# Optimization experiments

Measured on AMD Instinct MI355X. Metric: run time of the kernel, lower is better.

Reference implementation:

```python
import math
import jax, jax.numpy as jnp
import numpy as np

D = 512        # encoder_dim
LLM = 4096     # llm_dim
H = 8          # heads
L = 2          # depth
FF = 4 * D     # feedforward hidden
DH = D // H    # head dim
EPS = 1e-5


def setup_inputs() -> dict:
    key = jax.random.key(0)
    ks = jax.random.split(key, 16)
    s_d = 1.0 / math.sqrt(D)
    s_ff = 1.0 / math.sqrt(FF)
    inp = {
        "x": jax.random.normal(ks[0], (1, 8192, D), dtype=jnp.float32),
        # per-layer params, leading dim L
        "ln1_g": jnp.ones((L, D), jnp.float32),
        "ln1_b": jnp.zeros((L, D), jnp.float32),
        "Wq": jax.random.normal(ks[1], (L, D, D), jnp.float32) * s_d,
        "Wk": jax.random.normal(ks[2], (L, D, D), jnp.float32) * s_d,
        "Wv": jax.random.normal(ks[3], (L, D, D), jnp.float32) * s_d,
        "Wo": jax.random.normal(ks[4], (L, D, D), jnp.float32) * s_d,
        "bo": jnp.zeros((L, D), jnp.float32),
        "ln2_g": jnp.ones((L, D), jnp.float32),
        "ln2_b": jnp.zeros((L, D), jnp.float32),
        "W1": jax.random.normal(ks[5], (L, D, FF), jnp.float32) * s_d,
        "b1": jnp.zeros((L, FF), jnp.float32),
        "W2": jax.random.normal(ks[6], (L, FF, D), jnp.float32) * s_ff,
        "b2": jnp.zeros((L, D), jnp.float32),
        # final projector (xavier-like)
        "proj_W": jax.random.normal(ks[7], (D, LLM), jnp.float32) * math.sqrt(2.0 / (D + LLM)),
        "proj_b": jnp.zeros((LLM,), jnp.float32),
    }
    return inp


def _layernorm(h, g, b):
    mu = jnp.mean(h, axis=-1, keepdims=True)
    var = jnp.var(h, axis=-1, keepdims=True)
    return (h - mu) * jax.lax.rsqrt(var + EPS) * g + b


def _sinusoidal_pe(n, d):
    pos = jnp.arange(n, dtype=jnp.float32)[:, None]
    div = jnp.exp(jnp.arange(0, d, 2, dtype=jnp.float32) * (-math.log(10000.0) / d))
    pe = jnp.zeros((n, d), jnp.float32)
    pe = pe.at[:, 0::2].set(jnp.sin(pos * div))
    pe = pe.at[:, 1::2].set(jnp.cos(pos * div))
    return pe


def reference(x, ln1_g, ln1_b, Wq, Wk, Wv, Wo, bo, ln2_g, ln2_b, W1, b1, W2, b2, proj_W, proj_b):
    B, N, _ = x.shape
    x = x + _sinusoidal_pe(N, D)[None]  # positional encoding (dropout = identity at eval)
    scale = DH ** -0.5
    for l in range(L):
        # --- linear self-attention block (PreNorm + residual) ---
        h = _layernorm(x, ln1_g[l], ln1_b[l])
        q = (h @ Wq[l]).reshape(B, N, H, DH).transpose(0, 2, 1, 3)  # bhnd
        k = (h @ Wk[l]).reshape(B, N, H, DH).transpose(0, 2, 1, 3)
        v = (h @ Wv[l]).reshape(B, N, H, DH).transpose(0, 2, 1, 3)
        q = jax.nn.softmax(q, axis=-1) * scale        # softmax over feature dim
        k = jax.nn.softmax(k, axis=-2)                # softmax over sequence dim
        ctx = jnp.einsum('bhnd,bhne->bhde', k, v)     # small [B,H,DH,DH] context
        o = jnp.einsum('bhnd,bhde->bhne', q, ctx)
        o = o.transpose(0, 2, 1, 3).reshape(B, N, D)
        x = x + (o @ Wo[l] + bo[l])
        # --- feedforward block (PreNorm + residual, exact GELU) ---
        h = _layernorm(x, ln2_g[l], ln2_b[l])
        x = x + (jax.nn.gelu(h @ W1[l] + b1[l], approximate=False) @ W2[l] + b2[l])
    x = jnp.squeeze(x, 0)  # batch==1, matches torch x.squeeze(0)
    return x @ proj_W + proj_b  # [N, LLM]
```

## Files before the change

### kernel.cpp

```cpp
#include <hip/hip_runtime.h>
#include <hip/hip_bf16.h>
#include <math.h>

constexpr int N_SEQ = 8192;
constexpr int D     = 512;
constexpr int NH    = 8;
constexpr int FFDIM = 2048;
constexpr int LLMD  = 4096;
constexpr int NLAYER= 2;

typedef __bf16 bf16x8 __attribute__((ext_vector_type(8)));
typedef float  f32x4  __attribute__((ext_vector_type(4)));
typedef unsigned short u16x8 __attribute__((ext_vector_type(8)));

__device__ __forceinline__ unsigned short f2bf(float x) {
  unsigned u = __builtin_bit_cast(unsigned, x);
  unsigned r = (u + 0x7FFFu + ((u >> 16) & 1u)) >> 16;
  return (unsigned short)r;
}
__device__ __forceinline__ float bf2f(unsigned short u) {
  unsigned x = ((unsigned)u) << 16;
  return __builtin_bit_cast(float, x);
}

#define GLOAD16(g, l)                                                        \
  __builtin_amdgcn_global_load_lds(                                          \
      (const __attribute__((address_space(1))) void*)(g),                    \
      (__attribute__((address_space(3))) void*)(l), 16, 0, 0)

__global__ __launch_bounds__(256) void prep_kernel(const float* __restrict__ Wq,
                                                   const float* __restrict__ Wk,
                                                   const float* __restrict__ Wv,
                                                   const float* __restrict__ Wo,
                                                   const float* __restrict__ W1,
                                                   const float* __restrict__ W2,
                                                   const float* __restrict__ Wp,
                                                   unsigned short* __restrict__ WT,
                                                   const float* __restrict__ xin,
                                                   float* __restrict__ X,
                                                   unsigned short* __restrict__ Hb,
                                                   const float* __restrict__ g,
                                                   const float* __restrict__ b) {
  int bid = blockIdx.x;
  if (bid >= 8192) {
    int row  = ((bid - 8192) * 256 + (int)threadIdx.x) >> 6;
    int lane = threadIdx.x & 63;
    const float* p = xin + (size_t)row * D + lane * 8;
    float x[8];
#pragma unroll
    for (int i = 0; i < 8; ++i) {
      int d = lane * 8 + i;
      float freq = __expf((float)(d & ~1) * (-9.210340371976184f / 512.0f));
      float arg = (float)row * freq;
      float pe = (d & 1) ? cosf(arg) : sinf(arg);
      x[i] = p[i] + pe;
    }
    float s = 0.f, sq = 0.f;
#pragma unroll
    for (int i = 0; i < 8; ++i) { s += x[i]; sq += x[i] * x[i]; }
#pragma unroll
    for (int o = 32; o > 0; o >>= 1) { s += __shfl_xor(s, o); sq += __shfl_xor(sq, o); }
    float mu  = s * (1.0f / D);
    float var = sq * (1.0f / D) - mu * mu;
    float rs  = rsqrtf(var + 1e-5f);
    float* Xp = X + (size_t)row * D + lane * 8;
    u16x8 r;
#pragma unroll
    for (int i = 0; i < 8; ++i) {
      Xp[i] = x[i];
      r[i] = f2bf((x[i] - mu) * rs * g[lane * 8 + i] + b[lane * 8 + i]);
    }
    *(u16x8*)(Hb + (size_t)row * D + lane * 8) = r;
    return;
  }
  const float* src; unsigned short* dst; int K, N, tile;
  if (bid < 2048) {
    int mat = bid >> 8; int w = mat >> 1, l = mat & 1;
    const float* s4 = (w == 0) ? Wq : (w == 1) ? Wk : (w == 2) ? Wv : Wo;
    src = s4 + (size_t)l * 262144;
    dst = WT + ((size_t)l * 4 + w) * 262144;
    K = 512; N = 512; tile = bid & 255;
  } else if (bid < 4096) {
    int b2 = bid - 2048; int l = b2 >> 10;
    src = W1 + (size_t)l * 1048576; dst = WT + 2097152 + (size_t)l * 1048576;
    K = 512; N = 2048; tile = b2 & 1023;
  } else if (bid < 6144) {
    int b2 = bid - 4096; int l = b2 >> 10;
    src = W2 + (size_t)l * 1048576; dst = WT + 4194304 + (size_t)l * 1048576;
    K = 2048; N = 512; tile = b2 & 1023;
  } else {
    src = Wp; dst = WT + 6291456; K = 512; N = 4096; tile = bid - 6144;
  }
  int tilesN = N >> 5;
  int bk = (tile / tilesN) << 5, bn = (tile % tilesN) << 5;
  __shared__ float s[32][33];
  int r = threadIdx.x >> 5, c = threadIdx.x & 31;
#pragma unroll
  for (int i = 0; i < 4; ++i)
    s[r + 8 * i][c] = src[(size_t)(bk + r + 8 * i) * N + bn + c];
  __syncthreads();
#pragma unroll
  for (int i = 0; i < 4; ++i) {
    int rr = r + 8 * i;
    dst[(size_t)(bn + rr) * K + bk + c] = f2bf(s[c][rr]);
  }
}

__global__ __launch_bounds__(256) void ln_bf16(const float* __restrict__ in,
                                               unsigned short* __restrict__ out,
                                               const float* __restrict__ g,
                                               const float* __restrict__ b) {
  int row  = (blockIdx.x * 256 + threadIdx.x) >> 6;
  int lane = threadIdx.x & 63;
  const float* p = in + (size_t)row * D + lane * 8;
  f32x4 v0 = *(const f32x4*)p;
  f32x4 v1 = *(const f32x4*)(p + 4);
  float s  = v0[0] + v0[1] + v0[2] + v0[3] + v1[0] + v1[1] + v1[2] + v1[3];
  float sq = v0[0]*v0[0] + v0[1]*v0[1] + v0[2]*v0[2] + v0[3]*v0[3]
           + v1[0]*v1[0] + v1[1]*v1[1] + v1[2]*v1[2] + v1[3]*v1[3];
#pragma unroll
  for (int o = 32; o > 0; o >>= 1) { s += __shfl_xor(s, o); sq += __shfl_xor(sq, o); }
  float mu  = s * (1.0f / D);
  float var = sq * (1.0f / D) - mu * mu;
  float rs  = rsqrtf(var + 1e-5f);
  f32x4 g0 = *(const f32x4*)(g + lane * 8);
  f32x4 g1 = *(const f32x4*)(g + lane * 8 + 4);
  f32x4 b0 = *(const f32x4*)(b + lane * 8);
  f32x4 b1 = *(const f32x4*)(b + lane * 8 + 4);
  u16x8 r;
#pragma unroll
  for (int i = 0; i < 4; ++i) r[i]     = f2bf((v0[i] - mu) * rs * g0[i] + b0[i]);
#pragma unroll
  for (int i = 0; i < 4; ++i) r[i + 4] = f2bf((v1[i] - mu) * rs * g1[i] + b1[i]);
  *(u16x8*)(out + (size_t)row * D + lane * 8) = r;
}

template <int FLAGS, int BN>
__global__ __launch_bounds__(256) void mgemm2(const unsigned short* __restrict__ A,
                                              const unsigned short* __restrict__ Bt,
                                              const float* __restrict__ bias,
                                              const float* __restrict__ res,
                                              float* __restrict__ C,
                                              unsigned short* __restrict__ Cb,
                                              int M, int N, int K) {
  constexpr int WNI = BN / 32;
  __shared__ unsigned short As[4][128][32];
  __shared__ unsigned short Bs[4][BN][32];
  const int tid = threadIdx.x;
  const int lane = tid & 63, wv = tid >> 6;
  const int nwg = gridDim.x * gridDim.y;
  int bid = blockIdx.y * gridDim.x + blockIdx.x;
  bid = (bid & 7) * (nwg >> 3) + (bid >> 3);
  const int bm = (bid / gridDim.x) * 128, bn = (bid % gridDim.x) * BN;
  const int wr = (wv >> 1) * 64, wc = (wv & 1) * (BN / 2);
  f32x4 acc[4][WNI] = {};

  const int srA = wv * 32 + (lane >> 2);
  const int sc  = (lane & 3) * 8;
  const unsigned short* Ap0 = A + (size_t)(bm + srA) * K + sc;
  const unsigned short* Ap1 = Ap0 + (size_t)16 * K;
  const int srB = wv * (BN / 4) + (lane >> 2);
  const unsigned short* Bp0 = Bt + (size_t)(bn + srB) * K + sc;
  const unsigned short* Bp1 = Bp0 + (size_t)16 * K;
  const int kh = (lane >> 4) * 8;
  const int fr = lane & 15;

  auto stage = [&](int bb, int k0) {
    GLOAD16(Ap0 + k0, &As[bb][srA][sc]);
    GLOAD16(Ap1 + k0, &As[bb][srA + 16][sc]);
    GLOAD16(Bp0 + k0, &Bs[bb][srB][sc]);
    if constexpr (BN == 128) GLOAD16(Bp1 + k0, &Bs[bb][srB + 16][sc]);
  };

  const int nt = K >> 5;
  stage(0, 0);
  stage(1, 32);
  stage(2, 64);
  for (int t = 0; t < nt; ++t) {
    __builtin_amdgcn_sched_barrier(0);
    if constexpr (BN == 128)
      asm volatile("s_waitcnt vmcnt(8)" ::: "memory");
    else
      asm volatile("s_waitcnt vmcnt(6)" ::: "memory");
    __builtin_amdgcn_s_barrier();
    __builtin_amdgcn_sched_barrier(0);
    const int bb = t & 3;
    bf16x8 af[4], bfv[WNI];
#pragma unroll
    for (int mi = 0; mi < 4; ++mi)
      af[mi] = *(const bf16x8*)&As[bb][wr + mi * 16 + fr][kh];
#pragma unroll
    for (int ni = 0; ni < WNI; ++ni)
      bfv[ni] = *(const bf16x8*)&Bs[bb][wc + ni * 16 + fr][kh];
    if (t + 3 < nt) stage((t + 3) & 3, (t + 3) << 5);
#pragma unroll
    for (int mi = 0; mi < 4; ++mi)
#pragma unroll
      for (int ni = 0; ni < WNI; ++ni)
        acc[mi][ni] = __builtin_amdgcn_mfma_f32_16x16x32_bf16(af[mi], bfv[ni], acc[mi][ni], 0, 0, 0);
  }

  const int r4 = (lane >> 4) * 4, cc = lane & 15;
#pragma unroll
  for (int mi = 0; mi < 4; ++mi) {
#pragma unroll
    for (int ni = 0; ni < WNI; ++ni) {
      int col = bn + wc + ni * 16 + cc;
      float bsv = (FLAGS & 1) ? bias[col] : 0.0f;
      f32x4 v = acc[mi][ni];
#pragma unroll
      for (int j = 0; j < 4; ++j) {
        int row = bm + wr + mi * 16 + r4 + j;
        float x = v[j] + bsv;
        if (FLAGS & 2) x = 0.5f * x * (1.0f + erff(x * 0.7071067811865475f));
        if (FLAGS & 4) x += res[(size_t)row * N + col];
        if (!(FLAGS & 16)) C[(size_t)row * N + col] = x;
        if (FLAGS & 8) Cb[(size_t)row * N + col] = f2bf(x);
      }
    }
  }
}

__global__ __launch_bounds__(256) void qkv_gemm(const unsigned short* __restrict__ A,
                                                const unsigned short* __restrict__ Bt,
                                                unsigned short* __restrict__ Qb,
                                                unsigned short* __restrict__ Kb,
                                                unsigned short* __restrict__ Vb,
                                                float* __restrict__ pm,
                                                float* __restrict__ ps) {
  constexpr int K = 512;
  __shared__ unsigned short As[4][128][32];
  __shared__ unsigned short Bs[4][128][32];
  const int tid = threadIdx.x;
  const int lane = tid & 63, wv = tid >> 6;
  const int bm = blockIdx.y * 128, bn = blockIdx.x * 128;
  const int wr = (wv >> 1) * 64, wc = (wv & 1) * 64;
  f32x4 acc[4][4] = {};

  const int srA = wv * 32 + (lane >> 2);
  const int sc  = (lane & 3) * 8;
  const unsigned short* Ap0 = A + (size_t)(bm + srA) * K + sc;
  const unsigned short* Ap1 = Ap0 + (size_t)16 * K;
  const unsigned short* Bp0 = Bt + (size_t)(bn + srA) * K + sc;
  const unsigned short* Bp1 = Bp0 + (size_t)16 * K;
  const int kh = (lane >> 4) * 8;
  const int fr = lane & 15;

  auto stage = [&](int bb, int k0) {
    GLOAD16(Ap0 + k0, &As[bb][srA][sc]);
    GLOAD16(Ap1 + k0, &As[bb][srA + 16][sc]);
    GLOAD16(Bp0 + k0, &Bs[bb][srA][sc]);
    GLOAD16(Bp1 + k0, &Bs[bb][srA + 16][sc]);
  };

  stage(0, 0);
  stage(1, 32);
  stage(2, 64);
  for (int t = 0; t < 16; ++t) {
    __builtin_amdgcn_sched_barrier(0);
    asm volatile("s_waitcnt vmcnt(8)" ::: "memory");
    __builtin_amdgcn_s_barrier();
    __builtin_amdgcn_sched_barrier(0);
    const int bb = t & 3;
    bf16x8 af[4], bfv[4];
#pragma unroll
    for (int mi = 0; mi < 4; ++mi)
      af[mi] = *(const bf16x8*)&As[bb][wr + mi * 16 + fr][kh];
#pragma unroll
    for (int ni = 0; ni < 4; ++ni)
      bfv[ni] = *(const bf16x8*)&Bs[bb][wc + ni * 16 + fr][kh];
    if (t + 3 < 16) stage((t + 3) & 3, (t + 3) << 5);
#pragma unroll
    for (int mi = 0; mi < 4; ++mi)
#pragma unroll
      for (int ni = 0; ni < 4; ++ni)
        acc[mi][ni] = __builtin_amdgcn_mfma_f32_16x16x32_bf16(af[mi], bfv[ni], acc[mi][ni], 0, 0, 0);
  }

  const int r4 = (lane >> 4) * 4, cc = lane & 15;
  if (bn < 512) {
#pragma unroll
    for (int mi = 0; mi < 4; ++mi) {
#pragma unroll
      for (int j = 0; j < 4; ++j) {
        float v0 = acc[mi][0][j], v1 = acc[mi][1][j];
        float v2 = acc[mi][2][j], v3 = acc[mi][3][j];
        float m = fmaxf(fmaxf(v0, v1), fmaxf(v2, v3));
        m = fmaxf(m, __shfl_xor(m, 1)); m = fmaxf(m, __shfl_xor(m, 2));
        m = fmaxf(m, __shfl_xor(m, 4)); m = fmaxf(m, __shfl_xor(m, 8));
        float e0 = __expf(v0 - m), e1 = __expf(v1 - m);
        float e2 = __expf(v2 - m), e3 = __expf(v3 - m);
        float s = e0 + e1 + e2 + e3;
        s += __shfl_xor(s, 1); s += __shfl_xor(s, 2);
        s += __shfl_xor(s, 4); s += __shfl_xor(s, 8);
        float w = 0.125f / s;
        int row = bm + wr + mi * 16 + r4 + j;
        unsigned short* qr = Qb + (size_t)row * 512 + bn + wc + cc;
        qr[0] = f2bf(e0 * w); qr[16] = f2bf(e1 * w);
        qr[32] = f2bf(e2 * w); qr[48] = f2bf(e3 * w);
      }
    }
  } else if (bn < 1024) {
    int colb = bn - 512 + wc + cc;
    int prow = blockIdx.y * 2 + (wr ? 1 : 0);
#pragma unroll
    for (int ni = 0; ni < 4; ++ni) {
      float kf[4][4];
      float m = -1e30f;
#pragma unroll
      for (int mi = 0; mi < 4; ++mi)
#pragma unroll
        for (int j = 0; j < 4; ++j) {
          unsigned short kr = f2bf(acc[mi][ni][j]);
          Kb[(size_t)(bm + wr + mi * 16 + r4 + j) * 512 + colb + ni * 16] = kr;
          kf[mi][j] = bf2f(kr);
          m = fmaxf(m, kf[mi][j]);
        }
      m = fmaxf(m, __shfl_xor(m, 16));
      m = fmaxf(m, __shfl_xor(m, 32));
      float s = 0.f;
#pragma unroll
      for (int mi = 0; mi < 4; ++mi)
#pragma unroll
        for (int j = 0; j < 4; ++j) s += __expf(kf[mi][j] - m);
      s += __shfl_xor(s, 16);
      s += __shfl_xor(s, 32);
      if (lane < 16) {
        pm[(size_t)prow * 512 + colb + ni * 16] = m;
        ps[(size_t)prow * 512 + colb + ni * 16] = s;
      }
    }
  } else {
    int colv = bn - 1024 + wc + cc;
#pragma unroll
    for (int mi = 0; mi < 4; ++mi)
#pragma unroll
      for (int ni = 0; ni < 4; ++ni) {
        f32x4 v = acc[mi][ni];
#pragma unroll
        for (int j = 0; j < 4; ++j)
          Vb[(size_t)(bm + wr + mi * 16 + r4 + j) * 512 + colv + ni * 16] = f2bf(v[j]);
      }
  }
}

__global__ __launch_bounds__(256) void ctx_kernel(const unsigned short* __restrict__ kb,
                                                  const unsigned short* __restrict__ vb,
                                                  const float* __restrict__ pm,
                                                  const float* __restrict__ ps,
                                                  float* __restrict__ part) {
  int chunk = blockIdx.x, h = blockIdx.y, t = threadIdx.x;
  __shared__ float ks[64][64], vs[64][64];
  __shared__ float qm[4][64], qsum[4][64], scm[64], sci[64];
  {
    int c = t & 63, qt = t >> 6;
    float m = -1e30f, s = 0.f;
    for (int r = qt * 32; r < qt * 32 + 32; ++r) {
      float vm = pm[(size_t)r * 512 + h * 64 + c];
      float vp = ps[(size_t)r * 512 + h * 64 + c];
      float nm = fmaxf(m, vm);
      s = s * __expf(m - nm) + vp * __expf(vm - nm);
      m = nm;
    }
    qm[qt][c] = m; qsum[qt][c] = s;
  }
  __syncthreads();
  if (t < 64) {
    float M = fmaxf(fmaxf(qm[0][t], qm[1][t]), fmaxf(qm[2][t], qm[3][t]));
    float S = qsum[0][t] * __expf(qm[0][t] - M) + qsum[1][t] * __expf(qm[1][t] - M)
            + qsum[2][t] * __expf(qm[2][t] - M) + qsum[3][t] * __expf(qm[3][t] - M);
    scm[t] = M; sci[t] = 1.0f / S;
  }
  float acc[16] = {};
  int e0 = (t >> 6) * 16, dd = t & 63;
  for (int s0 = 0; s0 < 256; s0 += 64) {
    size_t rowbase = (size_t)chunk * 256 + s0;
    __syncthreads();
    for (int i = t; i < 1024; i += 256) {
      int r = i >> 4, c4 = (i & 15) * 4;
      ushort4 k4 = *(const ushort4*)&kb[(rowbase + r) * 512 + h * 64 + c4];
      ks[r][c4 + 0] = __expf(bf2f(k4.x) - scm[c4 + 0]) * sci[c4 + 0];
      ks[r][c4 + 1] = __expf(bf2f(k4.y) - scm[c4 + 1]) * sci[c4 + 1];
      ks[r][c4 + 2] = __expf(bf2f(k4.z) - scm[c4 + 2]) * sci[c4 + 2];
      ks[r][c4 + 3] = __expf(bf2f(k4.w) - scm[c4 + 3]) * sci[c4 + 3];
      ushort4 v4 = *(const ushort4*)&vb[(rowbase + r) * 512 + h * 64 + c4];
      vs[r][c4 + 0] = bf2f(v4.x); vs[r][c4 + 1] = bf2f(v4.y);
      vs[r][c4 + 2] = bf2f(v4.z); vs[r][c4 + 3] = bf2f(v4.w);
    }
    __syncthreads();
    for (int r = 0; r < 64; ++r) {
      float kd = ks[r][dd];
      float4 v0 = *(const float4*)&vs[r][e0];
      float4 v1 = *(const float4*)&vs[r][e0 + 4];
      float4 v2 = *(const float4*)&vs[r][e0 + 8];
      float4 v3 = *(const float4*)&vs[r][e0 + 12];
      acc[0]  = fmaf(kd, v0.x, acc[0]);  acc[1]  = fmaf(kd, v0.y, acc[1]);
      acc[2]  = fmaf(kd, v0.z, acc[2]);  acc[3]  = fmaf(kd, v0.w, acc[3]);
      acc[4]  = fmaf(kd, v1.x, acc[4]);  acc[5]  = fmaf(kd, v1.y, acc[5]);
      acc[6]  = fmaf(kd, v1.z, acc[6]);  acc[7]  = fmaf(kd, v1.w, acc[7]);
      acc[8]  = fmaf(kd, v2.x, acc[8]);  acc[9]  = fmaf(kd, v2.y, acc[9]);
      acc[10] = fmaf(kd, v2.z, acc[10]); acc[11] = fmaf(kd, v2.w, acc[11]);
      acc[12] = fmaf(kd, v3.x, acc[12]); acc[13] = fmaf(kd, v3.y, acc[13]);
      acc[14] = fmaf(kd, v3.z, acc[14]); acc[15] = fmaf(kd, v3.w, acc[15]);
    }
  }
  float* pb = &part[((size_t)h * 32 + chunk) * 4096 + dd * 64 + e0];
#pragma unroll
  for (int j = 0; j < 16; ++j) pb[j] = acc[j];
}

__global__ __launch_bounds__(256) void ctx_reduce_kernel(const float* __restrict__ part,
                                                         float* __restrict__ ctx) {
  int idx = blockIdx.x * 256 + threadIdx.x;
  int h = idx >> 12, de = idx & 4095;
  float s = 0.f;
#pragma unroll 8
  for (int c = 0; c < 32; ++c) s += part[((size_t)h * 32 + c) * 4096 + de];
  ctx[(size_t)h * 4096 + de] = s;
}

__global__ __launch_bounds__(256) void ctxw2_kernel(const float* __restrict__ ctx,
                                                    const float* __restrict__ Wo,
                                                    unsigned short* __restrict__ WPT) {
  int ct = blockIdx.x, h = blockIdx.y, t = threadIdx.x;
  __shared__ float cs[64][64];
  __shared__ float wo[64][64];
  for (int i = t; i < 4096; i += 256) {
    cs[i >> 6][i & 63] = ctx[(size_t)h * 4096 + i];
    wo[i >> 6][i & 63] = Wo[(size_t)(h * 64 + (i >> 6)) * 512 + ct * 64 + (i & 63)];
  }
  __syncthreads();
  int cl = t & 63, dg = (t >> 6) * 16;
  float accv[16];
#pragma unroll
  for (int j = 0; j < 16; ++j) accv[j] = 0.f;
  for (int e = 0; e < 64; ++e) {
    float w = wo[e][cl];
#pragma unroll
    for (int j = 0; j < 16; ++j) accv[j] = fmaf(cs[dg + j][e], w, accv[j]);
  }
  u16x8 o0, o1;
#pragma unroll
  for (int j = 0; j < 8; ++j) { o0[j] = f2bf(accv[j]); o1[j] = f2bf(accv[j + 8]); }
  unsigned short* dst = WPT + (size_t)(ct * 64 + cl) * 512 + h * 64 + dg;
  *(u16x8*)dst = o0;
  *(u16x8*)(dst + 8) = o1;
}

extern "C" void kernel_launch(void* const* d_in, const int* in_sizes, int n_in,
                              void* d_out, int out_size, void* d_ws, size_t ws_size,
                              hipStream_t stream) {
  const float* x_in  = (const float*)d_in[0];
  const float* ln1_g = (const float*)d_in[1];
  const float* ln1_b = (const float*)d_in[2];
  const float* Wq    = (const float*)d_in[3];
  const float* Wk    = (const float*)d_in[4];
  const float* Wv    = (const float*)d_in[5];
  const float* Wo    = (const float*)d_in[6];
  const float* bo    = (const float*)d_in[7];
  const float* ln2_g = (const float*)d_in[8];
  const float* ln2_b = (const float*)d_in[9];
  const float* W1    = (const float*)d_in[10];
  const float* b1    = (const float*)d_in[11];
  const float* W2    = (const float*)d_in[12];
  const float* b2    = (const float*)d_in[13];
  const float* projW = (const float*)d_in[14];
  const float* projb = (const float*)d_in[15];
  float* out = (float*)d_out;
  float* ws  = (float*)d_ws;
  constexpr size_t M1 = 1u << 20;

  float* X    = ws;
  float* CTXP = ws + 4 * M1;
  float* PM   = ws + 5 * M1;
  float* PS   = PM + 65536;
  float* CTX  = PS + 65536;
  unsigned short* Qb  = (unsigned short*)(ws + 6 * M1);
  unsigned short* Kb  = (unsigned short*)(ws + 8 * M1);
  unsigned short* Vb  = (unsigned short*)(ws + 10 * M1);
  unsigned short* Hb  = (unsigned short*)(ws + 12 * M1);
  unsigned short* Xb  = (unsigned short*)(ws + 14 * M1);
  unsigned short* FFH = (unsigned short*)(ws + 16 * M1);
  unsigned short* WT  = (unsigned short*)(ws + 24 * M1);
  unsigned short* WPT = (unsigned short*)(ws + 28 * M1);

  prep_kernel<<<10240, 256, 0, stream>>>(Wq, Wk, Wv, Wo, W1, W2, projW, WT,
                                         x_in, X, Hb, ln1_g, ln1_b);

  dim3 gqkv(1536 / 128, N_SEQ / 128);
  dim3 g512n(512 / 64, N_SEQ / 128);
  dim3 gff1(FFDIM / 128, N_SEQ / 128);
  dim3 gproj(LLMD / 128, N_SEQ / 128);

  for (int l = 0; l < NLAYER; ++l) {
    const unsigned short* WQKV = WT + (size_t)l * 1048576;
    const unsigned short* W1T  = WT + 2097152 + (size_t)l * 1048576;
    const unsigned short* W2T  = WT + 4194304 + (size_t)l * 1048576;

    qkv_gemm<<<gqkv, 256, 0, stream>>>(Hb, WQKV, Qb, Kb, Vb, PM, PS);
    ctx_kernel<<<dim3(32, NH), 256, 0, stream>>>(Kb, Vb, PM, PS, CTXP);
    ctx_reduce_kernel<<<128, 256, 0, stream>>>(CTXP, CTX);
    ctxw2_kernel<<<dim3(8, NH), 256, 0, stream>>>(CTX, Wo + (size_t)l * D * D, WPT);
    mgemm2<5, 64><<<g512n, 256, 0, stream>>>(Qb, WPT, bo + l * D, X, X, nullptr,
                                             N_SEQ, 512, 512);
    ln_bf16<<<N_SEQ / 4, 256, 0, stream>>>(X, Hb, ln2_g + l * D, ln2_b + l * D);
    mgemm2<27, 128><<<gff1, 256, 0, stream>>>(Hb, W1T, b1 + l * FFDIM, nullptr,
                                              nullptr, FFH, N_SEQ, FFDIM, 512);
    if (l == NLAYER - 1) {
      mgemm2<29, 64><<<g512n, 256, 0, stream>>>(FFH, W2T, b2 + l * D, X, nullptr,
                                                Xb, N_SEQ, 512, 2048);
    } else {
      mgemm2<5, 64><<<g512n, 256, 0, stream>>>(FFH, W2T, b2 + l * D, X, X, nullptr,
                                               N_SEQ, 512, 2048);
      ln_bf16<<<N_SEQ / 4, 256, 0, stream>>>(X, Hb, ln1_g + (l + 1) * D,
                                             ln1_b + (l + 1) * D);
    }
  }
  mgemm2<1, 128><<<gproj, 256, 0, stream>>>(Xb, WT + 6291456, projb, nullptr,
                                            out, nullptr, N_SEQ, LLMD, 512);
}
```

Measured before the change: 409.3 us.

## Use MFMA for ctx kernel and swizzle block order in qkv GEMM

The ctx kernel stages a whole 256-row chunk of softmaxed K and V into LDS as transposed, XOR-swizzled bf16 tiles. It then computes the 64x64 context with bf16 MFMA instructions instead of scalar fp32 FMAs. This replaces the fp32 LDS tiles and the loop of four staging steps with a single staging pass. Separately, the qkv_gemm block index is remapped so that workgroups are interleaved across eight groups, aiming for better cache or XCD locality. The softmaxed K is now rounded to bf16 before the product, which adds a small precision loss.

After: 383.5 us. 6.3% less time.

```diff
diff --git a/kernel.cpp b/kernel.cpp
--- a/kernel.cpp
+++ b/kernel.cpp
@@ -233,7 +233,11 @@
   __shared__ unsigned short Bs[4][128][32];
   const int tid = threadIdx.x;
   const int lane = tid & 63, wv = tid >> 6;
-  const int bm = blockIdx.y * 128, bn = blockIdx.x * 128;
+  const int nwg = gridDim.x * gridDim.y;
+  int bid = blockIdx.y * gridDim.x + blockIdx.x;
+  bid = (bid & 7) * (nwg >> 3) + (bid >> 3);
+  const int bm = (bid / gridDim.x) * 128, bn = (bid % gridDim.x) * 128;
+  const int bmy = bid / gridDim.x;
   const int wr = (wv >> 1) * 64, wc = (wv & 1) * 64;
   f32x4 acc[4][4] = {};
 
@@ -302,7 +306,7 @@
     }
   } else if (bn < 1024) {
     int colb = bn - 512 + wc + cc;
-    int prow = blockIdx.y * 2 + (wr ? 1 : 0);
+    int prow = bmy * 2 + (wr ? 1 : 0);
 #pragma unroll
     for (int ni = 0; ni < 4; ++ni) {
       float kf[4][4];
@@ -350,7 +354,8 @@
                                                   const float* __restrict__ ps,
                                                   float* __restrict__ part) {
   int chunk = blockIdx.x, h = blockIdx.y, t = threadIdx.x;
-  __shared__ float ks[64][64], vs[64][64];
+  __shared__ unsigned short kst[64 * 256];
+  __shared__ unsigned short vst[64 * 256];
   __shared__ float qm[4][64], qsum[4][64], scm[64], sci[64];
   {
     int c = t & 63, qt = t >> 6;
@@ -371,42 +376,50 @@
             + qsum[2][t] * __expf(qm[2][t] - M) + qsum[3][t] * __expf(qm[3][t] - M);
     scm[t] = M; sci[t] = 1.0f / S;
   }
-  float acc[16] = {};
-  int e0 = (t >> 6) * 16, dd = t & 63;
-  for (int s0 = 0; s0 < 256; s0 += 64) {
-    size_t rowbase = (size_t)chunk * 256 + s0;
-    __syncthreads();
-    for (int i = t; i < 1024; i += 256) {
-      int r = i >> 4, c4 = (i & 15) * 4;
-      ushort4 k4 = *(const ushort4*)&kb[(rowbase + r) * 512 + h * 64 + c4];
-      ks[r][c4 + 0] = __expf(bf2f(k4.x) - scm[c4 + 0]) * sci[c4 + 0];
-      ks[r][c4 + 1] = __expf(bf2f(k4.y) - scm[c4 + 1]) * sci[c4 + 1];
-      ks[r][c4 + 2] = __expf(bf2f(k4.z) - scm[c4 + 2]) * sci[c4 + 2];
-      ks[r][c4 + 3] = __expf(bf2f(k4.w) - scm[c4 + 3]) * sci[c4 + 3];
-      ushort4 v4 = *(const ushort4*)&vb[(rowbase + r) * 512 + h * 64 + c4];
-      vs[r][c4 + 0] = bf2f(v4.x); vs[r][c4 + 1] = bf2f(v4.y);
-      vs[r][c4 + 2] = bf2f(v4.z); vs[r][c4 + 3] = bf2f(v4.w);
-    }
-    __syncthreads();
-    for (int r = 0; r < 64; ++r) {
-      float kd = ks[r][dd];
-      float4 v0 = *(const float4*)&vs[r][e0];
-      float4 v1 = *(const float4*)&vs[r][e0 + 4];
-      float4 v2 = *(const float4*)&vs[r][e0 + 8];
-      float4 v3 = *(const float4*)&vs[r][e0 + 12];
-      acc[0]  = fmaf(kd, v0.x, acc[0]);  acc[1]  = fmaf(kd, v0.y, acc[1]);
-      acc[2]  = fmaf(kd, v0.z, acc[2]);  acc[3]  = fmaf(kd, v0.w, acc[3]);
-      acc[4]  = fmaf(kd, v1.x, acc[4]);  acc[5]  = fmaf(kd, v1.y, acc[5]);
-      acc[6]  = fmaf(kd, v1.z, acc[6]);  acc[7]  = fmaf(kd, v1.w, acc[7]);
-      acc[8]  = fmaf(kd, v2.x, acc[8]);  acc[9]  = fmaf(kd, v2.y, acc[9]);
-      acc[10] = fmaf(kd, v2.z, acc[10]); acc[11] = fmaf(kd, v2.w, acc[11]);
-      acc[12] = fmaf(kd, v3.x, acc[12]); acc[13] = fmaf(kd, v3.y, acc[13]);
-      acc[14] = fmaf(kd, v3.z, acc[14]); acc[15] = fmaf(kd, v3.w, acc[15]);
-    }
-  }
-  float* pb = &part[((size_t)h * 32 + chunk) * 4096 + dd * 64 + e0];
-#pragma unroll
-  for (int j = 0; j < 16; ++j) pb[j] = acc[j];
+  __syncthreads();
+  size_t rowbase = (size_t)chunk * 256;
+  for (int i = t; i < 4096; i += 256) {
+    int n = i >> 4, c4 = (i & 15) * 4;
+    ushort4 k4 = *(const ushort4*)&kb[(rowbase + n) * 512 + h * 64 + c4];
+    ushort4 v4 = *(const ushort4*)&vb[(rowbase + n) * 512 + h * 64 + c4];
+    unsigned short kr[4] = {
+      f2bf(__expf(bf2f(k4.x) - scm[c4 + 0]) * sci[c4 + 0]),
+      f2bf(__expf(bf2f(k4.y) - scm[c4 + 1]) * sci[c4 + 1]),
+      f2bf(__expf(bf2f(k4.z) - scm[c4 + 2]) * sci[c4 + 2]),
+      f2bf(__expf(bf2f(k4.w) - scm[c4 + 3]) * sci[c4 + 3])};
+    unsigned short vr[4] = {v4.x, v4.y, v4.z, v4.w};
+#pragma unroll
+    for (int j = 0; j < 4; ++j) {
+      int d = c4 + j;
+      int byt = (d * 512 + n * 2) ^ ((d & 7) << 4);
+      *(unsigned short*)((char*)kst + byt) = kr[j];
+      *(unsigned short*)((char*)vst + byt) = vr[j];
+    }
+  }
+  __syncthreads();
+  int lane = t & 63, wv = t >> 6;
+  int fr = lane & 15, kh = (lane >> 4) * 8;
+  f32x4 acc[4] = {};
+  int d = wv * 16 + fr;
+#pragma unroll
+  for (int kk = 0; kk < 8; ++kk) {
+    int abyt = (d * 512 + (kk * 32 + kh) * 2) ^ ((d & 7) << 4);
+    bf16x8 af = *(const bf16x8*)((const char*)kst + abyt);
+#pragma unroll
+    for (int ni = 0; ni < 4; ++ni) {
+      int e = ni * 16 + fr;
+      int bbyt = (e * 512 + (kk * 32 + kh) * 2) ^ ((e & 7) << 4);
+      bf16x8 bv = *(const bf16x8*)((const char*)vst + bbyt);
+      acc[ni] = __builtin_amdgcn_mfma_f32_16x16x32_bf16(af, bv, acc[ni], 0, 0, 0);
+    }
+  }
+  int r4 = (lane >> 4) * 4, cc = lane & 15;
+  float* pb = &part[((size_t)h * 32 + chunk) * 4096];
+#pragma unroll
+  for (int ni = 0; ni < 4; ++ni)
+#pragma unroll
+    for (int j = 0; j < 4; ++j)
+      pb[(wv * 16 + r4 + j) * 64 + ni * 16 + cc] = acc[ni][j];
 }
 
 __global__ __launch_bounds__(256) void ctx_reduce_kernel(const float* __restrict__ part,
```
